# Optimization experiments

Hardware: AMD Instinct MI355X
Metric: run time of the kernel (lower is better)

Reference implementation:

```python
import math
import jax, jax.numpy as jnp
import numpy as np

L, T, F, N_MIN, N_MAX = 16, 524288, 2, 16, 2048
DIM = 3
N_POINTS = 524288

# 8 corners of a 3D cell (matches cell_vert_offsets[3] in the original)
CELL_OFFSETS = jnp.asarray(
    [[0, 0, 0], [0, 0, 1], [0, 1, 0], [0, 1, 1],
     [1, 0, 0], [1, 0, 1], [1, 1, 0], [1, 1, 1]], dtype=jnp.float32)


def grid_meta():
    """Static (python) per-level metadata: scales, resolutions, first hash level, table offsets."""
    b = math.exp((math.log(N_MAX) - math.log(N_MIN)) / (L - 1))
    scales, resolutions, first_hash_level, offsets = [], [], 0, [0]
    for i in range(L):
        scale = N_MIN * b ** i - 1
        scales.append(scale)
        res = math.ceil(scale) + 1
        resolutions.append(res)
        n_entries = res ** DIM
        if n_entries <= T:
            first_hash_level += 1
        else:
            n_entries = T
        offsets.append(offsets[-1] + n_entries)
    return scales, resolutions, first_hash_level, offsets


def setup_inputs() -> dict:
    key = jax.random.key(0)
    k1, k2 = jax.random.split(key)
    _, _, _, offsets = grid_meta()
    pos = jax.random.uniform(k1, (N_POINTS, DIM), jnp.float32, -1.0, 1.0)
    # latent codes stored on grid vertices, init uniform(-1e-4, 1e-4) as in the module
    latents = jax.random.uniform(k2, (offsets[-1], F), jnp.float32, -1e-4, 1e-4)
    return {"pos": pos, "latents": latents, "bound": 1.0}


def _encode(pos, latents, bound):
    scales, resolutions, fhl, offsets = grid_meta()
    posn = (pos + bound) / (2 * bound)                      # [N,3] in [0,1]
    scales_a = jnp.asarray(scales, jnp.float32)             # [L]
    pos_scaled = posn[None, :, :] * scales_a[:, None, None] + 0.5   # [L,N,3]
    pos_floored = jnp.floor(pos_scaled)                     # [L,N,3]
    # integer positions of the 8 cell vertices, per level
    vert_pos = (pos_floored[:, :, None, :] + CELL_OFFSETS[None, None]).astype(jnp.uint32)  # [L,N,8,3]

    # tiled (dense) indices for coarse levels: idx = x + y*res + z*res^2
    res_t = jnp.asarray(resolutions[:fhl], jnp.uint32)      # [fhl]
    strides = jnp.stack([jnp.ones_like(res_t), res_t, res_t * res_t], axis=-1)  # [fhl,3]
    idx_tiled = jnp.sum(vert_pos[:fhl] * strides[:, None, None, :], axis=-1)    # [fhl,N,8]

    # spatial-hash indices for fine levels (uint32 wraparound multiply, as in NGP)
    p1 = jnp.uint32(2654435761)
    p2 = jnp.uint32(805459861)
    vh = vert_pos[fhl:]                                      # [L-fhl,N,8,3]
    idx_hash = vh[..., 0] ^ (vh[..., 1] * p1) ^ (vh[..., 2] * p2)

    indices = jnp.concatenate([idx_tiled, idx_hash], axis=0)        # [L,N,8]
    indices = jnp.mod(indices, jnp.uint32(T))
    indices = indices + jnp.asarray(offsets[:-1], jnp.uint32)[:, None, None]

    vert_latents = latents[indices]                          # [L,N,8,F] gather

    # multilinear interpolation weights
    pos_off = pos_scaled - pos_floored                       # fractional part (modf), [L,N,3]
    co = CELL_OFFSETS[None, None]                            # [1,1,8,3]
    widths = jnp.clip(1.0 - co + (2.0 * co - 1.0) * pos_off[:, :, None, :], 0.0, 1.0)
    weights = jnp.prod(widths, axis=-1)                      # [L,N,8]

    enc = (vert_latents * weights[..., None]).sum(axis=-2)   # [L,N,F]
    enc = enc.transpose(1, 0, 2).reshape(-1, L * F)          # [N, L*F]
    return enc


def reference(pos, latents, bound):
    enc = _encode(pos, latents, bound)
    tv = jnp.float32(0.0)   # tv_scale == 0 branch of the original
    return enc, tv
```

## Files before the change

kernel.cpp:

```cpp
#include <hip/hip_runtime.h>
#include <math.h>

#define NLEVELS 16
#define TBLSIZE 524288u
#define NPTS    524288
#define OUT_ENC_ELEMS (NPTS * NLEVELS * 2)

typedef float f32x2 __attribute__((ext_vector_type(2)));
typedef float f32x4 __attribute__((ext_vector_type(4)));

struct LevelMeta {
    float scale[NLEVELS];
    unsigned int res[NLEVELS];
    unsigned int off[NLEVELS];
    unsigned int fhl;
};

__global__ __launch_bounds__(256, 4) void hashgrid_encode_kernel(
    const float* __restrict__ pos,
    const float* __restrict__ latents,
    const float* __restrict__ bound_p,
    float* __restrict__ out,
    LevelMeta meta)
{
    const unsigned int point = blockIdx.x * 256u + threadIdx.x;

    const float bound = bound_p[0];
    const float denom = 2.0f * bound;

    const float px = (pos[point * 3 + 0] + bound) / denom;
    const float py = (pos[point * 3 + 1] + bound) / denom;
    const float pz = (pos[point * 3 + 2] + bound) / denom;

    const unsigned int p1 = 2654435761u;
    const unsigned int p2 = 805459861u;
    const f32x2* __restrict__ lat2 = (const f32x2*)latents;

    f32x2 acc[NLEVELS];

#pragma unroll
    for (int l = 0; l < NLEVELS; ++l) {
        const float scale = meta.scale[l];
        const unsigned int res = meta.res[l];
        const unsigned int off = meta.off[l];
        const bool hashed = ((unsigned int)l >= meta.fhl);

        const float sx = __fadd_rn(__fmul_rn(px, scale), 0.5f);
        const float sy = __fadd_rn(__fmul_rn(py, scale), 0.5f);
        const float sz = __fadd_rn(__fmul_rn(pz, scale), 0.5f);

        const float fx = floorf(sx);
        const float fy = floorf(sy);
        const float fz = floorf(sz);

        const float ox = __fsub_rn(sx, fx);
        const float oy = __fsub_rn(sy, fy);
        const float oz = __fsub_rn(sz, fz);

        const unsigned int bx = (unsigned int)fx;
        const unsigned int by = (unsigned int)fy;
        const unsigned int bz = (unsigned int)fz;

        float acc0 = 0.0f;
        float acc1 = 0.0f;

#pragma unroll
        for (int c = 0; c < 8; ++c) {
            const unsigned int c0 = (c >> 2) & 1;
            const unsigned int c1 = (c >> 1) & 1;
            const unsigned int c2 = c & 1;
            const unsigned int vx = bx + c0;
            const unsigned int vy = by + c1;
            const unsigned int vz = bz + c2;

            unsigned int idx_t = vx + vy * res + vz * res * res;
            unsigned int idx_h = vx ^ (vy * p1) ^ (vz * p2);
            unsigned int idx = (hashed ? idx_h : idx_t) & (TBLSIZE - 1u);
            idx += off;

            const float wx = c0 ? ox : (1.0f - ox);
            const float wy = c1 ? oy : (1.0f - oy);
            const float wz = c2 ? oz : (1.0f - oz);
            const float w = wx * wy * wz;

            const f32x2 v = lat2[idx];
            acc0 += v.x * w;
            acc1 += v.y * w;
        }

        acc[l].x = acc0;
        acc[l].y = acc1;

        __syncthreads();
        __builtin_amdgcn_sched_barrier(0);
    }

    f32x4* __restrict__ o4 = (f32x4*)(out + (size_t)point * (NLEVELS * 2));
#pragma unroll
    for (int i = 0; i < 8; ++i) {
        f32x4 v;
        v.x = acc[2 * i].x;
        v.y = acc[2 * i].y;
        v.z = acc[2 * i + 1].x;
        v.w = acc[2 * i + 1].y;
        __builtin_nontemporal_store(v, &o4[i]);
    }

    if (point == 0) {
        out[OUT_ENC_ELEMS] = 0.0f;
    }
}

extern "C" void kernel_launch(void* const* d_in, const int* in_sizes, int n_in,
                              void* d_out, int out_size, void* d_ws, size_t ws_size,
                              hipStream_t stream) {
    const float* pos     = (const float*)d_in[0];
    const float* latents = (const float*)d_in[1];
    const float* bound_p = (const float*)d_in[2];
    float* out = (float*)d_out;

    LevelMeta meta;
    const double b = exp((log(2048.0) - log(16.0)) / 15.0);
    unsigned int off = 0;
    unsigned int fhl = 0;
    for (int i = 0; i < NLEVELS; ++i) {
        const double scale = 16.0 * pow(b, (double)i) - 1.0;
        meta.scale[i] = (float)scale;
        const unsigned int res = (unsigned int)ceil(scale) + 1u;
        meta.res[i] = res;
        unsigned int n_entries = res * res * res;
        if (n_entries <= TBLSIZE) {
            fhl = (unsigned int)(i + 1);
        } else {
            n_entries = TBLSIZE;
        }
        meta.off[i] = off;
        off += n_entries;
    }
    meta.fhl = fhl;

    const int block = 256;
    const int grid = NPTS / block;
    hipLaunchKernelGGL(hashgrid_encode_kernel, dim3(grid), dim3(block), 0, stream,
                       pos, latents, bound_p, out, meta);
}
```

Before: 506.4 us.

## Split encoding into per-level hash kernels with workspace staging and pack pass

Instead of one kernel handling all 16 levels per point, the dense levels run in one kernel and each hashed level runs in its own launch, writing results to a level-major workspace. A final pack kernel transposes the workspace into the point-major output. The aim is that only one hash level's table (about 4 MB) is live at a time, so it can stay resident in L2/cache, rather than all levels competing for cache. The cost is many extra launches, a round trip of 64 MB through workspace, and the pos input being reread by every launch. The old single-kernel path remains as a fallback when the workspace is too small.

```diff
diff --git a/kernel.cpp b/kernel.cpp
--- a/kernel.cpp
+++ b/kernel.cpp
@@ -16,7 +16,133 @@
     unsigned int fhl;
 };
 
-__global__ __launch_bounds__(256, 4) void hashgrid_encode_kernel(
+__device__ __forceinline__ void norm_point(const float* __restrict__ pos,
+                                           const float* __restrict__ bound_p,
+                                           unsigned int point,
+                                           float& px, float& py, float& pz)
+{
+    const float bound = bound_p[0];
+    const float denom = 2.0f * bound;
+    px = (pos[point * 3 + 0] + bound) / denom;
+    py = (pos[point * 3 + 1] + bound) / denom;
+    pz = (pos[point * 3 + 2] + bound) / denom;
+}
+
+__global__ __launch_bounds__(256) void tiled_levels_kernel(
+    const float* __restrict__ pos,
+    const float* __restrict__ latents,
+    const float* __restrict__ bound_p,
+    f32x2* __restrict__ ws,
+    LevelMeta meta)
+{
+    const unsigned int point = blockIdx.x * 256u + threadIdx.x;
+    float px, py, pz;
+    norm_point(pos, bound_p, point, px, py, pz);
+
+    const f32x2* __restrict__ lat2 = (const f32x2*)latents;
+
+    for (unsigned int l = 0; l < meta.fhl; ++l) {
+        const float scale = meta.scale[l];
+        const unsigned int res = meta.res[l];
+        const unsigned int off = meta.off[l];
+
+        const float sx = __fadd_rn(__fmul_rn(px, scale), 0.5f);
+        const float sy = __fadd_rn(__fmul_rn(py, scale), 0.5f);
+        const float sz = __fadd_rn(__fmul_rn(pz, scale), 0.5f);
+        const float fx = floorf(sx), fy = floorf(sy), fz = floorf(sz);
+        const float ox = __fsub_rn(sx, fx);
+        const float oy = __fsub_rn(sy, fy);
+        const float oz = __fsub_rn(sz, fz);
+        const unsigned int bx = (unsigned int)fx;
+        const unsigned int by = (unsigned int)fy;
+        const unsigned int bz = (unsigned int)fz;
+
+        float acc0 = 0.0f, acc1 = 0.0f;
+#pragma unroll
+        for (int c = 0; c < 8; ++c) {
+            const unsigned int c0 = (c >> 2) & 1;
+            const unsigned int c1 = (c >> 1) & 1;
+            const unsigned int c2 = c & 1;
+            unsigned int idx = ((bx + c0) + (by + c1) * res + (bz + c2) * res * res)
+                               & (TBLSIZE - 1u);
+            idx += off;
+            const float wx = c0 ? ox : (1.0f - ox);
+            const float wy = c1 ? oy : (1.0f - oy);
+            const float wz = c2 ? oz : (1.0f - oz);
+            const float w = wx * wy * wz;
+            const f32x2 v = lat2[idx];
+            acc0 += v.x * w;
+            acc1 += v.y * w;
+        }
+        f32x2 r; r.x = acc0; r.y = acc1;
+        ws[(size_t)l * NPTS + point] = r;
+    }
+}
+
+__global__ __launch_bounds__(256) void hash_level_kernel(
+    const float* __restrict__ pos,
+    const float* __restrict__ latents,
+    const float* __restrict__ bound_p,
+    f32x2* __restrict__ ws,
+    float scale, unsigned int off, unsigned int l)
+{
+    const unsigned int point = blockIdx.x * 256u + threadIdx.x;
+    float px, py, pz;
+    norm_point(pos, bound_p, point, px, py, pz);
+
+    const unsigned int p1 = 2654435761u;
+    const unsigned int p2 = 805459861u;
+    const f32x2* __restrict__ lat2 = (const f32x2*)latents;
+
+    const float sx = __fadd_rn(__fmul_rn(px, scale), 0.5f);
+    const float sy = __fadd_rn(__fmul_rn(py, scale), 0.5f);
+    const float sz = __fadd_rn(__fmul_rn(pz, scale), 0.5f);
+    const float fx = floorf(sx), fy = floorf(sy), fz = floorf(sz);
+    const float ox = __fsub_rn(sx, fx);
+    const float oy = __fsub_rn(sy, fy);
+    const float oz = __fsub_rn(sz, fz);
+    const unsigned int bx = (unsigned int)fx;
+    const unsigned int by = (unsigned int)fy;
+    const unsigned int bz = (unsigned int)fz;
+
+    float acc0 = 0.0f, acc1 = 0.0f;
+#pragma unroll
+    for (int c = 0; c < 8; ++c) {
+        const unsigned int c0 = (c >> 2) & 1;
+        const unsigned int c1 = (c >> 1) & 1;
+        const unsigned int c2 = c & 1;
+        unsigned int idx = ((bx + c0) ^ ((by + c1) * p1) ^ ((bz + c2) * p2))
+                           & (TBLSIZE - 1u);
+        idx += off;
+        const float wx = c0 ? ox : (1.0f - ox);
+        const float wy = c1 ? oy : (1.0f - oy);
+        const float wz = c2 ? oz : (1.0f - oz);
+        const float w = wx * wy * wz;
+        const f32x2 v = lat2[idx];
+        acc0 += v.x * w;
+        acc1 += v.y * w;
+    }
+    f32x2 r; r.x = acc0; r.y = acc1;
+    ws[(size_t)l * NPTS + point] = r;
+}
+
+__global__ __launch_bounds__(256) void pack_kernel(
+    const f32x2* __restrict__ ws,
+    float* __restrict__ out)
+{
+    const unsigned int point = blockIdx.x * 256u + threadIdx.x;
+    f32x4* __restrict__ o4 = (f32x4*)(out + (size_t)point * (NLEVELS * 2));
+#pragma unroll
+    for (int i = 0; i < 8; ++i) {
+        const f32x2 a = ws[(size_t)(2 * i) * NPTS + point];
+        const f32x2 b = ws[(size_t)(2 * i + 1) * NPTS + point];
+        f32x4 v; v.x = a.x; v.y = a.y; v.z = b.x; v.w = b.y;
+        __builtin_nontemporal_store(v, &o4[i]);
+    }
+    if (point == 0) out[OUT_ENC_ELEMS] = 0.0f;
+}
+
+__global__ __launch_bounds__(256, 4) void hashgrid_encode_fallback(
     const float* __restrict__ pos,
     const float* __restrict__ latents,
     const float* __restrict__ bound_p,
@@ -24,18 +150,12 @@
     LevelMeta meta)
 {
     const unsigned int point = blockIdx.x * 256u + threadIdx.x;
-
-    const float bound = bound_p[0];
-    const float denom = 2.0f * bound;
-
-    const float px = (pos[point * 3 + 0] + bound) / denom;
-    const float py = (pos[point * 3 + 1] + bound) / denom;
-    const float pz = (pos[point * 3 + 2] + bound) / denom;
+    float px, py, pz;
+    norm_point(pos, bound_p, point, px, py, pz);
 
     const unsigned int p1 = 2654435761u;
     const unsigned int p2 = 805459861u;
     const f32x2* __restrict__ lat2 = (const f32x2*)latents;
-
     f32x2 acc[NLEVELS];
 
 #pragma unroll
@@ -48,22 +168,15 @@
         const float sx = __fadd_rn(__fmul_rn(px, scale), 0.5f);
         const float sy = __fadd_rn(__fmul_rn(py, scale), 0.5f);
         const float sz = __fadd_rn(__fmul_rn(pz, scale), 0.5f);
-
-        const float fx = floorf(sx);
-        const float fy = floorf(sy);
-        const float fz = floorf(sz);
-
+        const float fx = floorf(sx), fy = floorf(sy), fz = floorf(sz);
         const float ox = __fsub_rn(sx, fx);
         const float oy = __fsub_rn(sy, fy);
         const float oz = __fsub_rn(sz, fz);
-
         const unsigned int bx = (unsigned int)fx;
         const unsigned int by = (unsigned int)fy;
         const unsigned int bz = (unsigned int)fz;
 
-        float acc0 = 0.0f;
-        float acc1 = 0.0f;
-
+        float a0 = 0.0f, a1 = 0.0f;
 #pragma unroll
         for (int c = 0; c < 8; ++c) {
             const unsigned int c0 = (c >> 2) & 1;
@@ -72,25 +185,19 @@
             const unsigned int vx = bx + c0;
             const unsigned int vy = by + c1;
             const unsigned int vz = bz + c2;
-
             unsigned int idx_t = vx + vy * res + vz * res * res;
             unsigned int idx_h = vx ^ (vy * p1) ^ (vz * p2);
             unsigned int idx = (hashed ? idx_h : idx_t) & (TBLSIZE - 1u);
             idx += off;
-
             const float wx = c0 ? ox : (1.0f - ox);
             const float wy = c1 ? oy : (1.0f - oy);
             const float wz = c2 ? oz : (1.0f - oz);
             const float w = wx * wy * wz;
-
             const f32x2 v = lat2[idx];
-            acc0 += v.x * w;
-            acc1 += v.y * w;
-        }
-
-        acc[l].x = acc0;
-        acc[l].y = acc1;
-
+            a0 += v.x * w;
+            a1 += v.y * w;
+        }
+        acc[l].x = a0; acc[l].y = a1;
         __syncthreads();
         __builtin_amdgcn_sched_barrier(0);
     }
@@ -99,16 +206,11 @@
 #pragma unroll
     for (int i = 0; i < 8; ++i) {
         f32x4 v;
-        v.x = acc[2 * i].x;
-        v.y = acc[2 * i].y;
-        v.z = acc[2 * i + 1].x;
-        v.w = acc[2 * i + 1].y;
+        v.x = acc[2 * i].x;   v.y = acc[2 * i].y;
+        v.z = acc[2 * i + 1].x; v.w = acc[2 * i + 1].y;
         __builtin_nontemporal_store(v, &o4[i]);
     }
-
-    if (point == 0) {
-        out[OUT_ENC_ELEMS] = 0.0f;
-    }
+    if (point == 0) out[OUT_ENC_ELEMS] = 0.0f;
 }
 
 extern "C" void kernel_launch(void* const* d_in, const int* in_sizes, int n_in,
@@ -141,6 +243,20 @@
 
     const int block = 256;
     const int grid = NPTS / block;
-    hipLaunchKernelGGL(hashgrid_encode_kernel, dim3(grid), dim3(block), 0, stream,
-                       pos, latents, bound_p, out, meta);
-}
+    const size_t ws_needed = (size_t)NLEVELS * NPTS * sizeof(float) * 2;
+
+    if (ws_size >= ws_needed) {
+        f32x2* ws = (f32x2*)d_ws;
+        hipLaunchKernelGGL(tiled_levels_kernel, dim3(grid), dim3(block), 0, stream,
+                           pos, latents, bound_p, ws, meta);
+        for (unsigned int l = fhl; l < NLEVELS; ++l) {
+            hipLaunchKernelGGL(hash_level_kernel, dim3(grid), dim3(block), 0, stream,
+                               pos, latents, bound_p, ws,
+                               meta.scale[l], meta.off[l], l);
+        }
+        hipLaunchKernelGGL(pack_kernel, dim3(grid), dim3(block), 0, stream, ws, out);
+    } else {
+        hipLaunchKernelGGL(hashgrid_encode_fallback, dim3(grid), dim3(block), 0, stream,
+                           pos, latents, bound_p, out, meta);
+    }
+}
```

Result: slower. 539.4 us (+6.5%).

## Split hashed levels into per-level kernels writing to workspace, then pack

Applied to the files above, without the earlier changes.

Computes each hashed level in its own kernel launch, so every launch gathers from a single 4 MB hash table slice that fits in cache. Results go to a workspace plane per level. A final kernel computes the dense coarse levels, reads the workspace planes and writes the packed output. The aim is better L2/MALL locality for the random gathers. The cost is 12 launches, about 44 MB of extra workspace traffic, and reloading the positions in every launch.

```diff
diff --git a/kernel.cpp b/kernel.cpp
--- a/kernel.cpp
+++ b/kernel.cpp
@@ -5,6 +5,7 @@
 #define TBLSIZE 524288u
 #define NPTS    524288
 #define OUT_ENC_ELEMS (NPTS * NLEVELS * 2)
+#define FHL_EXPECTED 5u
 
 typedef float f32x2 __attribute__((ext_vector_type(2)));
 typedef float f32x4 __attribute__((ext_vector_type(4)));
@@ -16,7 +17,122 @@
     unsigned int fhl;
 };
 
-__global__ __launch_bounds__(256, 4) void hashgrid_encode_kernel(
+__device__ __forceinline__ void norm_point(const float* __restrict__ pos,
+                                           const float* __restrict__ bound_p,
+                                           unsigned int point,
+                                           float& px, float& py, float& pz)
+{
+    const float bound = bound_p[0];
+    const float denom = 2.0f * bound;
+    px = (pos[point * 3 + 0] + bound) / denom;
+    py = (pos[point * 3 + 1] + bound) / denom;
+    pz = (pos[point * 3 + 2] + bound) / denom;
+}
+
+template<bool HASHED>
+__device__ __forceinline__ f32x2 level_interp(
+    const f32x2* __restrict__ lat2,
+    float px, float py, float pz,
+    float scale, unsigned int res, unsigned int off)
+{
+    const unsigned int p1 = 2654435761u;
+    const unsigned int p2 = 805459861u;
+
+    const float sx = __fadd_rn(__fmul_rn(px, scale), 0.5f);
+    const float sy = __fadd_rn(__fmul_rn(py, scale), 0.5f);
+    const float sz = __fadd_rn(__fmul_rn(pz, scale), 0.5f);
+    const float fx = floorf(sx), fy = floorf(sy), fz = floorf(sz);
+    const float ox = __fsub_rn(sx, fx);
+    const float oy = __fsub_rn(sy, fy);
+    const float oz = __fsub_rn(sz, fz);
+    const unsigned int bx = (unsigned int)fx;
+    const unsigned int by = (unsigned int)fy;
+    const unsigned int bz = (unsigned int)fz;
+
+    float acc0 = 0.0f, acc1 = 0.0f;
+#pragma unroll
+    for (int c = 0; c < 8; ++c) {
+        const unsigned int c0 = (c >> 2) & 1;
+        const unsigned int c1 = (c >> 1) & 1;
+        const unsigned int c2 = c & 1;
+        const unsigned int vx = bx + c0;
+        const unsigned int vy = by + c1;
+        const unsigned int vz = bz + c2;
+        unsigned int idx;
+        if (HASHED) idx = (vx ^ (vy * p1) ^ (vz * p2)) & (TBLSIZE - 1u);
+        else        idx = (vx + vy * res + vz * res * res) & (TBLSIZE - 1u);
+        idx += off;
+        const float wx = c0 ? ox : (1.0f - ox);
+        const float wy = c1 ? oy : (1.0f - oy);
+        const float wz = c2 ? oz : (1.0f - oz);
+        const float w = wx * wy * wz;
+        const f32x2 v = lat2[idx];
+        acc0 += v.x * w;
+        acc1 += v.y * w;
+    }
+    f32x2 r; r.x = acc0; r.y = acc1;
+    return r;
+}
+
+__global__ __launch_bounds__(256) void hash_level_kernel(
+    const float* __restrict__ pos,
+    const float* __restrict__ latents,
+    const float* __restrict__ bound_p,
+    f32x2* __restrict__ ws_plane,
+    float scale, unsigned int off)
+{
+    const unsigned int t = blockIdx.x * 256u + threadIdx.x;
+    const f32x2* __restrict__ lat2 = (const f32x2*)latents;
+
+#pragma unroll
+    for (int k = 0; k < 2; ++k) {
+        const unsigned int point = t + (unsigned int)k * (NPTS / 2);
+        float px, py, pz;
+        norm_point(pos, bound_p, point, px, py, pz);
+        ws_plane[point] = level_interp<true>(lat2, px, py, pz, scale, 0u, off);
+    }
+}
+
+__global__ __launch_bounds__(256) void pack_tiled_kernel(
+    const float* __restrict__ pos,
+    const float* __restrict__ latents,
+    const float* __restrict__ bound_p,
+    const f32x2* __restrict__ ws,
+    float* __restrict__ out,
+    LevelMeta meta)
+{
+    const unsigned int point = blockIdx.x * 256u + threadIdx.x;
+    const f32x2* __restrict__ lat2 = (const f32x2*)latents;
+
+    float px, py, pz;
+    norm_point(pos, bound_p, point, px, py, pz);
+
+    f32x2 acc[NLEVELS];
+
+#pragma unroll
+    for (int l = FHL_EXPECTED; l < NLEVELS; ++l) {
+        acc[l] = __builtin_nontemporal_load(
+            &ws[(size_t)(l - FHL_EXPECTED) * NPTS + point]);
+    }
+
+#pragma unroll
+    for (int l = 0; l < (int)FHL_EXPECTED; ++l) {
+        acc[l] = level_interp<false>(lat2, px, py, pz,
+                                     meta.scale[l], meta.res[l], meta.off[l]);
+    }
+
+    f32x4* __restrict__ o4 = (f32x4*)(out + (size_t)point * (NLEVELS * 2));
+#pragma unroll
+    for (int i = 0; i < 8; ++i) {
+        f32x4 v;
+        v.x = acc[2 * i].x;     v.y = acc[2 * i].y;
+        v.z = acc[2 * i + 1].x; v.w = acc[2 * i + 1].y;
+        o4[i] = v;
+    }
+    if (point == 0) out[OUT_ENC_ELEMS] = 0.0f;
+}
+
+__global__ __launch_bounds__(256, 4) void hashgrid_encode_fallback(
     const float* __restrict__ pos,
     const float* __restrict__ latents,
     const float* __restrict__ bound_p,
@@ -24,73 +140,17 @@
     LevelMeta meta)
 {
     const unsigned int point = blockIdx.x * 256u + threadIdx.x;
-
-    const float bound = bound_p[0];
-    const float denom = 2.0f * bound;
-
-    const float px = (pos[point * 3 + 0] + bound) / denom;
-    const float py = (pos[point * 3 + 1] + bound) / denom;
-    const float pz = (pos[point * 3 + 2] + bound) / denom;
-
-    const unsigned int p1 = 2654435761u;
-    const unsigned int p2 = 805459861u;
     const f32x2* __restrict__ lat2 = (const f32x2*)latents;
+    float px, py, pz;
+    norm_point(pos, bound_p, point, px, py, pz);
 
     f32x2 acc[NLEVELS];
-
 #pragma unroll
     for (int l = 0; l < NLEVELS; ++l) {
-        const float scale = meta.scale[l];
-        const unsigned int res = meta.res[l];
-        const unsigned int off = meta.off[l];
         const bool hashed = ((unsigned int)l >= meta.fhl);
-
-        const float sx = __fadd_rn(__fmul_rn(px, scale), 0.5f);
-        const float sy = __fadd_rn(__fmul_rn(py, scale), 0.5f);
-        const float sz = __fadd_rn(__fmul_rn(pz, scale), 0.5f);
-
-        const float fx = floorf(sx);
-        const float fy = floorf(sy);
-        const float fz = floorf(sz);
-
-        const float ox = __fsub_rn(sx, fx);
-        const float oy = __fsub_rn(sy, fy);
-        const float oz = __fsub_rn(sz, fz);
-
-        const unsigned int bx = (unsigned int)fx;
-        const unsigned int by = (unsigned int)fy;
-        const unsigned int bz = (unsigned int)fz;
-
-        float acc0 = 0.0f;
-        float acc1 = 0.0f;
-
-#pragma unroll
-        for (int c = 0; c < 8; ++c) {
-            const unsigned int c0 = (c >> 2) & 1;
-            const unsigned int c1 = (c >> 1) & 1;
-            const unsigned int c2 = c & 1;
-            const unsigned int vx = bx + c0;
-            const unsigned int vy = by + c1;
-            const unsigned int vz = bz + c2;
-
-            unsigned int idx_t = vx + vy * res + vz * res * res;
-            unsigned int idx_h = vx ^ (vy * p1) ^ (vz * p2);
-            unsigned int idx = (hashed ? idx_h : idx_t) & (TBLSIZE - 1u);
-            idx += off;
-
-            const float wx = c0 ? ox : (1.0f - ox);
-            const float wy = c1 ? oy : (1.0f - oy);
-            const float wz = c2 ? oz : (1.0f - oz);
-            const float w = wx * wy * wz;
-
-            const f32x2 v = lat2[idx];
-            acc0 += v.x * w;
-            acc1 += v.y * w;
-        }
-
-        acc[l].x = acc0;
-        acc[l].y = acc1;
-
+        acc[l] = hashed
+            ? level_interp<true>(lat2, px, py, pz, meta.scale[l], meta.res[l], meta.off[l])
+            : level_interp<false>(lat2, px, py, pz, meta.scale[l], meta.res[l], meta.off[l]);
         __syncthreads();
         __builtin_amdgcn_sched_barrier(0);
     }
@@ -99,16 +159,11 @@
 #pragma unroll
     for (int i = 0; i < 8; ++i) {
         f32x4 v;
-        v.x = acc[2 * i].x;
-        v.y = acc[2 * i].y;
-        v.z = acc[2 * i + 1].x;
-        v.w = acc[2 * i + 1].y;
-        __builtin_nontemporal_store(v, &o4[i]);
-    }
-
-    if (point == 0) {
-        out[OUT_ENC_ELEMS] = 0.0f;
-    }
+        v.x = acc[2 * i].x;     v.y = acc[2 * i].y;
+        v.z = acc[2 * i + 1].x; v.w = acc[2 * i + 1].y;
+        o4[i] = v;
+    }
+    if (point == 0) out[OUT_ENC_ELEMS] = 0.0f;
 }
 
 extern "C" void kernel_launch(void* const* d_in, const int* in_sizes, int n_in,
@@ -140,7 +195,24 @@
     meta.fhl = fhl;
 
     const int block = 256;
-    const int grid = NPTS / block;
-    hipLaunchKernelGGL(hashgrid_encode_kernel, dim3(grid), dim3(block), 0, stream,
-                       pos, latents, bound_p, out, meta);
-}
+    const size_t ws_needed =
+        (size_t)(NLEVELS - FHL_EXPECTED) * NPTS * sizeof(float) * 2;
+
+    if (fhl == FHL_EXPECTED && ws_size >= ws_needed) {
+        f32x2* ws = (f32x2*)d_ws;
+        const int hgrid = (NPTS / 2) / block;
+        for (unsigned int l = fhl; l < NLEVELS; ++l) {
+            hipLaunchKernelGGL(hash_level_kernel, dim3(hgrid), dim3(block), 0, stream,
+                               pos, latents, bound_p,
+                               ws + (size_t)(l - fhl) * NPTS,
+                               meta.scale[l], meta.off[l]);
+        }
+        const int pgrid = NPTS / block;
+        hipLaunchKernelGGL(pack_tiled_kernel, dim3(pgrid), dim3(block), 0, stream,
+                           pos, latents, bound_p, ws, out, meta);
+    } else {
+        const int grid = NPTS / block;
+        hipLaunchKernelGGL(hashgrid_encode_fallback, dim3(grid), dim3(block), 0, stream,
+                           pos, latents, bound_p, out, meta);
+    }
+}
```

New measurement: 421.2 us. 16.8% less time.
